# Kernel tuning notes

Measured on AMD Instinct MI355X. Metric: run time of the kernel, lower is better.

The kernel has to match this reference:

```python
import jax, jax.numpy as jnp
import numpy as np

LOG2 = float(np.log(2.0))
NEG_INF = float('-inf')


def log1mexp(x):
    # numerically accurate log(1 - exp(x)) for x < 0
    return jnp.where(x > -LOG2, jnp.log(-jnp.expm1(x)), jnp.log1p(-jnp.exp(x)))


def encode_input_log(pos):
    neg = log1mexp(pos)
    # interleave [pos_i, neg_i] then prepend constants [-inf (log 0), 0 (log 1)]
    result = jnp.stack([pos, neg], axis=1).reshape(-1)
    constants = jnp.array([NEG_INF, 0.0], dtype=pos.dtype)
    return jnp.concatenate([constants, result])


def sum_layer(x, ptrs, csr, n):
    # product node in log semiring: segment-sum of gathered log-values
    return jax.ops.segment_sum(x[ptrs], csr, num_segments=n)


def logsum_layer(x, ptrs, csr, n, epsilon=1e-15):
    # sum node in log semiring: numerically stable segment log-sum-exp
    g = x[ptrs]
    m = jax.lax.stop_gradient(jax.ops.segment_max(g, csr, num_segments=n))
    z = g - m[csr]
    z = jnp.nan_to_num(z, nan=0.0, posinf=jnp.inf, neginf=-jnp.inf)  # (-inf)-(-inf) -> 0
    s = jax.ops.segment_sum(jnp.exp(z), csr, num_segments=n) + epsilon
    return jnp.log(s) + m


def setup_inputs() -> dict:
    key = jax.random.key(0)
    n_vars = 2_000_000
    deg = 4
    Ns = [4_000_000, 2_000_000, 1_000_000, 500_000]
    sizes_in = [2 + 2 * n_vars] + Ns[:-1]
    ks = jax.random.split(key, 1 + len(Ns))
    # log-probabilities strictly in (log eps, log(1-eps)) so log1mexp is finite
    u = jax.random.uniform(ks[0], (n_vars,), dtype=jnp.float32, minval=1e-6, maxval=1.0 - 1e-6)
    inp = {"weights": jnp.log(u)}
    for i, n in enumerate(Ns):
        e = n * deg
        inp[f"ptrs{i}"] = jax.random.randint(ks[i + 1], (e,), 0, sizes_in[i], dtype=jnp.int32)
        inp[f"csr{i}"] = jnp.repeat(jnp.arange(n, dtype=jnp.int32), deg)  # unrolled CSR, fan-in=deg
        inp[f"n{i}"] = n
    return inp


def reference(weights, ptrs0, csr0, ptrs1, csr1, ptrs2, csr2, ptrs3, csr3, n0, n1, n2, n3):
    x = encode_input_log(weights)
    x = sum_layer(x, ptrs0, csr0, n0)      # layer 0: product (even)
    x = logsum_layer(x, ptrs1, csr1, n1)   # layer 1: sum (odd)
    x = sum_layer(x, ptrs2, csr2, n2)      # layer 2: product
    x = logsum_layer(x, ptrs3, csr3, n3)   # layer 3: sum
    return x
```

## Files before the change

### kernel.cpp

```cpp
#include <hip/hip_runtime.h>
#include <math.h>

#define NEG_INF (-INFINITY)

typedef int      v4i __attribute__((ext_vector_type(4)));
typedef float    v4f __attribute__((ext_vector_type(4)));
typedef _Float16 v4h __attribute__((ext_vector_type(4)));

__device__ __forceinline__ float fast_log1mexp(float v) {
    if (v > -0.125f) {
        float e = v * (1.0f + v * (0.5f + v * (0.16666667f + v * 0.041666667f)));
        return __logf(-e);
    }
    return __logf(1.0f - __expf(v));
}

__global__ __launch_bounds__(256) void cvt_kernel(const float* __restrict__ w,
                                                  _Float16* __restrict__ wh, int n) {
    int i = blockIdx.x * blockDim.x + threadIdx.x;
    int n4 = n >> 2;
    if (i < n4) {
        v4f v = reinterpret_cast<const v4f*>(w)[i];
        v4h o;
        o.x = (_Float16)v.x; o.y = (_Float16)v.y;
        o.z = (_Float16)v.z; o.w = (_Float16)v.w;
        reinterpret_cast<v4h*>(wh)[i] = o;
    }
    int base = n4 << 2;
    if (i < (n - base)) wh[base + i] = (_Float16)w[base + i];
}

__device__ __forceinline__ int widx(int p) { int j = (p >> 1) - 1; return j < 0 ? 0 : j; }
__device__ __forceinline__ float fixw(int p, float v) {
    float r = (p & 1) ? fast_log1mexp(v) : v;
    if (p < 2) r = (p == 0) ? NEG_INF : 0.0f;
    return r;
}

__global__ __launch_bounds__(256) void sum4_enc_kernel(const _Float16* __restrict__ wh,
                                                       const v4i* __restrict__ ptrs,
                                                       _Float16* __restrict__ y, int n, int h) {
    int t = blockIdx.x * blockDim.x + threadIdx.x;
    if (t >= h) return;
    int i0 = t, i1 = t + h, i2 = t + 2 * h, i3 = t + 3 * h;
    int c1 = i1 < n ? i1 : 0, c2 = i2 < n ? i2 : 0, c3 = i3 < n ? i3 : 0;
    v4i p0 = __builtin_nontemporal_load(ptrs + i0);
    v4i p1 = __builtin_nontemporal_load(ptrs + c1);
    v4i p2 = __builtin_nontemporal_load(ptrs + c2);
    v4i p3 = __builtin_nontemporal_load(ptrs + c3);
    float g00 = (float)wh[widx(p0.x)], g01 = (float)wh[widx(p0.y)];
    float g02 = (float)wh[widx(p0.z)], g03 = (float)wh[widx(p0.w)];
    float g10 = (float)wh[widx(p1.x)], g11 = (float)wh[widx(p1.y)];
    float g12 = (float)wh[widx(p1.z)], g13 = (float)wh[widx(p1.w)];
    float g20 = (float)wh[widx(p2.x)], g21 = (float)wh[widx(p2.y)];
    float g22 = (float)wh[widx(p2.z)], g23 = (float)wh[widx(p2.w)];
    float g30 = (float)wh[widx(p3.x)], g31 = (float)wh[widx(p3.y)];
    float g32 = (float)wh[widx(p3.z)], g33 = (float)wh[widx(p3.w)];
    float s0 = (fixw(p0.x, g00) + fixw(p0.y, g01)) + (fixw(p0.z, g02) + fixw(p0.w, g03));
    float s1 = (fixw(p1.x, g10) + fixw(p1.y, g11)) + (fixw(p1.z, g12) + fixw(p1.w, g13));
    float s2 = (fixw(p2.x, g20) + fixw(p2.y, g21)) + (fixw(p2.z, g22) + fixw(p2.w, g23));
    float s3 = (fixw(p3.x, g30) + fixw(p3.y, g31)) + (fixw(p3.z, g32) + fixw(p3.w, g33));
    __builtin_nontemporal_store((_Float16)s0, y + i0);
    if (i1 < n) __builtin_nontemporal_store((_Float16)s1, y + i1);
    if (i2 < n) __builtin_nontemporal_store((_Float16)s2, y + i2);
    if (i3 < n) __builtin_nontemporal_store((_Float16)s3, y + i3);
}

__device__ __forceinline__ float lse4(float a, float b, float c, float d) {
    float m = fmaxf(fmaxf(a, b), fmaxf(c, d));
    if (m == NEG_INF) return NEG_INF;
    float s = __expf(a - m) + __expf(b - m) + __expf(c - m) + __expf(d - m) + 1e-15f;
    return __logf(s) + m;
}

__global__ __launch_bounds__(256) void logsum4_l1_kernel(const _Float16* __restrict__ x,
                                                         const v4i* __restrict__ ptrs,
                                                         _Float16* __restrict__ y,
                                                         int n, int h) {
    int t = blockIdx.x * blockDim.x + threadIdx.x;
    if (t >= h) return;
    int i0 = t, i1 = t + h;
    int c1 = i1 < n ? i1 : 0;
    v4i p0 = __builtin_nontemporal_load(ptrs + i0);
    v4i p1 = __builtin_nontemporal_load(ptrs + c1);
    float a0 = (float)x[p0.x], b0 = (float)x[p0.y];
    float e0 = (float)x[p0.z], d0 = (float)x[p0.w];
    float a1 = (float)x[p1.x], b1 = (float)x[p1.y];
    float e1 = (float)x[p1.z], d1 = (float)x[p1.w];
    float s0 = lse4(a0, b0, e0, d0);
    float s1 = lse4(a1, b1, e1, d1);
    __builtin_nontemporal_store((_Float16)s0, y + i0);
    if (i1 < n) __builtin_nontemporal_store((_Float16)s1, y + i1);
}

__global__ __launch_bounds__(256) void sum4_h2h_kernel(const _Float16* __restrict__ x,
                                                       const v4i* __restrict__ ptrs,
                                                       _Float16* __restrict__ y, int n, int h) {
    int t = blockIdx.x * blockDim.x + threadIdx.x;
    if (t >= h) return;
    int i0 = t, i1 = t + h;
    int c1 = i1 < n ? i1 : 0;
    v4i p0 = __builtin_nontemporal_load(ptrs + i0);
    v4i p1 = __builtin_nontemporal_load(ptrs + c1);
    float s0 = ((float)x[p0.x] + (float)x[p0.y]) + ((float)x[p0.z] + (float)x[p0.w]);
    float s1 = ((float)x[p1.x] + (float)x[p1.y]) + ((float)x[p1.z] + (float)x[p1.w]);
    __builtin_nontemporal_store((_Float16)s0, y + i0);
    if (i1 < n) __builtin_nontemporal_store((_Float16)s1, y + i1);
}

__global__ __launch_bounds__(256) void logsum4_h2f_kernel(const _Float16* __restrict__ x,
                                                          const v4i* __restrict__ ptrs,
                                                          float* __restrict__ y, int n) {
    int t = blockIdx.x * blockDim.x + threadIdx.x;
    if (t >= n) return;
    v4i p = __builtin_nontemporal_load(ptrs + t);
    float r = lse4((float)x[p.x], (float)x[p.y], (float)x[p.z], (float)x[p.w]);
    __builtin_nontemporal_store(r, y + t);
}

extern "C" void kernel_launch(void* const* d_in, const int* in_sizes, int n_in,
                              void* d_out, int out_size, void* d_ws, size_t ws_size,
                              hipStream_t stream) {
    const float* w     = (const float*)d_in[0];
    const v4i*   ptrs0 = (const v4i*)d_in[1];
    const v4i*   ptrs1 = (const v4i*)d_in[4];
    const v4i*   ptrs2 = (const v4i*)d_in[7];
    const v4i*   ptrs3 = (const v4i*)d_in[10];

    const int n_vars = in_sizes[0];
    const int n0 = in_sizes[1] / 4;
    const int n1 = in_sizes[4] / 4;
    const int n2 = in_sizes[7] / 4;
    const int n3 = in_sizes[10] / 4;

    char* ws = (char*)d_ws;
    size_t off = 0;
    _Float16* wh = (_Float16*)(ws + off); off += ((size_t)n_vars * 2 + 255) & ~(size_t)255;
    _Float16* y0 = (_Float16*)(ws + off); off += ((size_t)n0 * 2 + 255) & ~(size_t)255;
    _Float16* y1 = (_Float16*)(ws + off); off += ((size_t)n1 * 2 + 255) & ~(size_t)255;
    _Float16* y2 = (_Float16*)(ws + off);
    float* out = (float*)d_out;

    const int B = 256;
    int hc = (n_vars + 3) / 4;
    int h0 = (n0 + 3) / 4;
    int h1 = (n1 + 1) / 2;
    int h2 = (n2 + 1) / 2;

    cvt_kernel        <<<(hc + B - 1) / B, B, 0, stream>>>(w, wh, n_vars);
    sum4_enc_kernel   <<<(h0 + B - 1) / B, B, 0, stream>>>(wh, ptrs0, y0, n0, h0);
    logsum4_l1_kernel <<<(h1 + B - 1) / B, B, 0, stream>>>(y0, ptrs1, y1, n1, h1);
    sum4_h2h_kernel   <<<(h2 + B - 1) / B, B, 0, stream>>>(y1, ptrs2, y2, n2, h2);
    logsum4_h2f_kernel<<<(n3 + B - 1) / B, B, 0, stream>>>(y2, ptrs3, out, n3);
}
```

Measured before the change: 371.1 us.

## Split layer-1 gathers into two index-range passes to improve cache locality

The layer-1 logsum kernel now gives each thread four output nodes instead of two. It gathers inputs in two phases: first only the pointers into the lower half of the layer-0 output, then, after a block barrier, the pointers into the upper half. The two partial log-sum-exps are combined with a merge step. The aim is to keep each phase's random-gather working set (about 4 MB of fp16) resident in cache, in exchange for extra predicated loads and exp/log work, a __syncthreads that only loosely aligns phases across the grid, and launch bounds of 8 waves.

```diff
diff --git a/kernel.cpp b/kernel.cpp
--- a/kernel.cpp
+++ b/kernel.cpp
@@ -66,31 +66,84 @@
     if (i3 < n) __builtin_nontemporal_store((_Float16)s3, y + i3);
 }
 
-__device__ __forceinline__ float lse4(float a, float b, float c, float d) {
+__device__ __forceinline__ float plse4(float a, float b, float c, float d) {
     float m = fmaxf(fmaxf(a, b), fmaxf(c, d));
     if (m == NEG_INF) return NEG_INF;
-    float s = __expf(a - m) + __expf(b - m) + __expf(c - m) + __expf(d - m) + 1e-15f;
+    float s = __expf(a - m) + __expf(b - m) + __expf(c - m) + __expf(d - m);
     return __logf(s) + m;
 }
 
-__global__ __launch_bounds__(256) void logsum4_l1_kernel(const _Float16* __restrict__ x,
-                                                         const v4i* __restrict__ ptrs,
-                                                         _Float16* __restrict__ y,
-                                                         int n, int h) {
-    int t = blockIdx.x * blockDim.x + threadIdx.x;
-    if (t >= h) return;
-    int i0 = t, i1 = t + h;
-    int c1 = i1 < n ? i1 : 0;
+__device__ __forceinline__ float merge_lse(float LA, float LB) {
+    float m = fmaxf(LA, LB);
+    if (m == NEG_INF) return NEG_INF;
+    float s = __expf(LA - m) + __expf(LB - m) + 1e-15f;
+    return __logf(s) + m;
+}
+
+__global__ __launch_bounds__(256, 8) void l1_fused_kernel(const _Float16* __restrict__ x,
+                                                          const v4i* __restrict__ ptrs,
+                                                          _Float16* __restrict__ y,
+                                                          int n, int h, int half) {
+    int t = blockIdx.x * blockDim.x + threadIdx.x;
+    bool act = t < h;
+    int tt = act ? t : 0;
+    int i0 = tt, i1 = tt + h, i2 = tt + 2 * h, i3 = tt + 3 * h;
+    int c1 = i1 < n ? i1 : 0, c2 = i2 < n ? i2 : 0, c3 = i3 < n ? i3 : 0;
     v4i p0 = __builtin_nontemporal_load(ptrs + i0);
     v4i p1 = __builtin_nontemporal_load(ptrs + c1);
-    float a0 = (float)x[p0.x], b0 = (float)x[p0.y];
-    float e0 = (float)x[p0.z], d0 = (float)x[p0.w];
-    float a1 = (float)x[p1.x], b1 = (float)x[p1.y];
-    float e1 = (float)x[p1.z], d1 = (float)x[p1.w];
-    float s0 = lse4(a0, b0, e0, d0);
-    float s1 = lse4(a1, b1, e1, d1);
-    __builtin_nontemporal_store((_Float16)s0, y + i0);
-    if (i1 < n) __builtin_nontemporal_store((_Float16)s1, y + i1);
+    v4i p2 = __builtin_nontemporal_load(ptrs + c2);
+    v4i p3 = __builtin_nontemporal_load(ptrs + c3);
+
+    float a0 = p0.x < half ? (float)x[p0.x] : NEG_INF;
+    float b0 = p0.y < half ? (float)x[p0.y] : NEG_INF;
+    float e0 = p0.z < half ? (float)x[p0.z] : NEG_INF;
+    float d0 = p0.w < half ? (float)x[p0.w] : NEG_INF;
+    float a1 = p1.x < half ? (float)x[p1.x] : NEG_INF;
+    float b1 = p1.y < half ? (float)x[p1.y] : NEG_INF;
+    float e1 = p1.z < half ? (float)x[p1.z] : NEG_INF;
+    float d1 = p1.w < half ? (float)x[p1.w] : NEG_INF;
+    float a2 = p2.x < half ? (float)x[p2.x] : NEG_INF;
+    float b2 = p2.y < half ? (float)x[p2.y] : NEG_INF;
+    float e2 = p2.z < half ? (float)x[p2.z] : NEG_INF;
+    float d2 = p2.w < half ? (float)x[p2.w] : NEG_INF;
+    float a3 = p3.x < half ? (float)x[p3.x] : NEG_INF;
+    float b3 = p3.y < half ? (float)x[p3.y] : NEG_INF;
+    float e3 = p3.z < half ? (float)x[p3.z] : NEG_INF;
+    float d3 = p3.w < half ? (float)x[p3.w] : NEG_INF;
+    float la0 = plse4(a0, b0, e0, d0);
+    float la1 = plse4(a1, b1, e1, d1);
+    float la2 = plse4(a2, b2, e2, d2);
+    float la3 = plse4(a3, b3, e3, d3);
+
+    __syncthreads();
+
+    a0 = p0.x >= half ? (float)x[p0.x] : NEG_INF;
+    b0 = p0.y >= half ? (float)x[p0.y] : NEG_INF;
+    e0 = p0.z >= half ? (float)x[p0.z] : NEG_INF;
+    d0 = p0.w >= half ? (float)x[p0.w] : NEG_INF;
+    a1 = p1.x >= half ? (float)x[p1.x] : NEG_INF;
+    b1 = p1.y >= half ? (float)x[p1.y] : NEG_INF;
+    e1 = p1.z >= half ? (float)x[p1.z] : NEG_INF;
+    d1 = p1.w >= half ? (float)x[p1.w] : NEG_INF;
+    a2 = p2.x >= half ? (float)x[p2.x] : NEG_INF;
+    b2 = p2.y >= half ? (float)x[p2.y] : NEG_INF;
+    e2 = p2.z >= half ? (float)x[p2.z] : NEG_INF;
+    d2 = p2.w >= half ? (float)x[p2.w] : NEG_INF;
+    a3 = p3.x >= half ? (float)x[p3.x] : NEG_INF;
+    b3 = p3.y >= half ? (float)x[p3.y] : NEG_INF;
+    e3 = p3.z >= half ? (float)x[p3.z] : NEG_INF;
+    d3 = p3.w >= half ? (float)x[p3.w] : NEG_INF;
+    float s0 = merge_lse(la0, plse4(a0, b0, e0, d0));
+    float s1 = merge_lse(la1, plse4(a1, b1, e1, d1));
+    float s2 = merge_lse(la2, plse4(a2, b2, e2, d2));
+    float s3 = merge_lse(la3, plse4(a3, b3, e3, d3));
+
+    if (act) {
+        __builtin_nontemporal_store((_Float16)s0, y + i0);
+        if (i1 < n) __builtin_nontemporal_store((_Float16)s1, y + i1);
+        if (i2 < n) __builtin_nontemporal_store((_Float16)s2, y + i2);
+        if (i3 < n) __builtin_nontemporal_store((_Float16)s3, y + i3);
+    }
 }
 
 __global__ __launch_bounds__(256) void sum4_h2h_kernel(const _Float16* __restrict__ x,
@@ -108,6 +161,13 @@
     if (i1 < n) __builtin_nontemporal_store((_Float16)s1, y + i1);
 }
 
+__device__ __forceinline__ float lse4(float a, float b, float c, float d) {
+    float m = fmaxf(fmaxf(a, b), fmaxf(c, d));
+    if (m == NEG_INF) return NEG_INF;
+    float s = __expf(a - m) + __expf(b - m) + __expf(c - m) + __expf(d - m) + 1e-15f;
+    return __logf(s) + m;
+}
+
 __global__ __launch_bounds__(256) void logsum4_h2f_kernel(const _Float16* __restrict__ x,
                                                           const v4i* __restrict__ ptrs,
                                                           float* __restrict__ y, int n) {
@@ -144,12 +204,13 @@
     const int B = 256;
     int hc = (n_vars + 3) / 4;
     int h0 = (n0 + 3) / 4;
-    int h1 = (n1 + 1) / 2;
+    int h1 = (n1 + 3) / 4;
     int h2 = (n2 + 1) / 2;
+    int half0 = n0 / 2;
 
     cvt_kernel        <<<(hc + B - 1) / B, B, 0, stream>>>(w, wh, n_vars);
     sum4_enc_kernel   <<<(h0 + B - 1) / B, B, 0, stream>>>(wh, ptrs0, y0, n0, h0);
-    logsum4_l1_kernel <<<(h1 + B - 1) / B, B, 0, stream>>>(y0, ptrs1, y1, n1, h1);
+    l1_fused_kernel   <<<(h1 + B - 1) / B, B, 0, stream>>>(y0, ptrs1, y1, n1, h1, half0);
     sum4_h2h_kernel   <<<(h2 + B - 1) / B, B, 0, stream>>>(y1, ptrs2, y2, n2, h2);
     logsum4_h2f_kernel<<<(n3 + B - 1) / B, B, 0, stream>>>(y2, ptrs3, out, n3);
 }
```

Measured after the change: 353.8 us. 4.7% less time.

## Fuse all layers into a cooperative persistent kernel with split-half gathers

Applied to the files above, without the earlier changes.

Replaces the five separate layer kernels with one cooperative kernel that uses grid-wide syncs between stages. The sum layer over y0 is split into two passes, each gathering only from one half of y0 and merging partial log-sum-exps, so each pass's gather working set is smaller and more cache-friendly. This removes per-launch overhead and aims to improve cache locality for random gathers. In exchange it adds several grid-wide barriers, doubles gather instruction count in that layer, and limits the grid to the resident block count.

```diff
diff --git a/kernel.cpp b/kernel.cpp
--- a/kernel.cpp
+++ b/kernel.cpp
@@ -1,7 +1,10 @@
 #include <hip/hip_runtime.h>
+#include <hip/hip_cooperative_groups.h>
 #include <math.h>
 
 #define NEG_INF (-INFINITY)
+
+namespace cg = cooperative_groups;
 
 typedef int      v4i __attribute__((ext_vector_type(4)));
 typedef float    v4f __attribute__((ext_vector_type(4)));
@@ -13,21 +16,6 @@
         return __logf(-e);
     }
     return __logf(1.0f - __expf(v));
-}
-
-__global__ __launch_bounds__(256) void cvt_kernel(const float* __restrict__ w,
-                                                  _Float16* __restrict__ wh, int n) {
-    int i = blockIdx.x * blockDim.x + threadIdx.x;
-    int n4 = n >> 2;
-    if (i < n4) {
-        v4f v = reinterpret_cast<const v4f*>(w)[i];
-        v4h o;
-        o.x = (_Float16)v.x; o.y = (_Float16)v.y;
-        o.z = (_Float16)v.z; o.w = (_Float16)v.w;
-        reinterpret_cast<v4h*>(wh)[i] = o;
-    }
-    int base = n4 << 2;
-    if (i < (n - base)) wh[base + i] = (_Float16)w[base + i];
 }
 
 __device__ __forceinline__ int widx(int p) { int j = (p >> 1) - 1; return j < 0 ? 0 : j; }
@@ -37,33 +25,18 @@
     return r;
 }
 
-__global__ __launch_bounds__(256) void sum4_enc_kernel(const _Float16* __restrict__ wh,
-                                                       const v4i* __restrict__ ptrs,
-                                                       _Float16* __restrict__ y, int n, int h) {
-    int t = blockIdx.x * blockDim.x + threadIdx.x;
-    if (t >= h) return;
-    int i0 = t, i1 = t + h, i2 = t + 2 * h, i3 = t + 3 * h;
-    int c1 = i1 < n ? i1 : 0, c2 = i2 < n ? i2 : 0, c3 = i3 < n ? i3 : 0;
-    v4i p0 = __builtin_nontemporal_load(ptrs + i0);
-    v4i p1 = __builtin_nontemporal_load(ptrs + c1);
-    v4i p2 = __builtin_nontemporal_load(ptrs + c2);
-    v4i p3 = __builtin_nontemporal_load(ptrs + c3);
-    float g00 = (float)wh[widx(p0.x)], g01 = (float)wh[widx(p0.y)];
-    float g02 = (float)wh[widx(p0.z)], g03 = (float)wh[widx(p0.w)];
-    float g10 = (float)wh[widx(p1.x)], g11 = (float)wh[widx(p1.y)];
-    float g12 = (float)wh[widx(p1.z)], g13 = (float)wh[widx(p1.w)];
-    float g20 = (float)wh[widx(p2.x)], g21 = (float)wh[widx(p2.y)];
-    float g22 = (float)wh[widx(p2.z)], g23 = (float)wh[widx(p2.w)];
-    float g30 = (float)wh[widx(p3.x)], g31 = (float)wh[widx(p3.y)];
-    float g32 = (float)wh[widx(p3.z)], g33 = (float)wh[widx(p3.w)];
-    float s0 = (fixw(p0.x, g00) + fixw(p0.y, g01)) + (fixw(p0.z, g02) + fixw(p0.w, g03));
-    float s1 = (fixw(p1.x, g10) + fixw(p1.y, g11)) + (fixw(p1.z, g12) + fixw(p1.w, g13));
-    float s2 = (fixw(p2.x, g20) + fixw(p2.y, g21)) + (fixw(p2.z, g22) + fixw(p2.w, g23));
-    float s3 = (fixw(p3.x, g30) + fixw(p3.y, g31)) + (fixw(p3.z, g32) + fixw(p3.w, g33));
-    __builtin_nontemporal_store((_Float16)s0, y + i0);
-    if (i1 < n) __builtin_nontemporal_store((_Float16)s1, y + i1);
-    if (i2 < n) __builtin_nontemporal_store((_Float16)s2, y + i2);
-    if (i3 < n) __builtin_nontemporal_store((_Float16)s3, y + i3);
+__device__ __forceinline__ float plse4(float a, float b, float c, float d) {
+    float m = fmaxf(fmaxf(a, b), fmaxf(c, d));
+    if (m == NEG_INF) return NEG_INF;
+    float s = __expf(a - m) + __expf(b - m) + __expf(c - m) + __expf(d - m);
+    return __logf(s) + m;
+}
+
+__device__ __forceinline__ float merge_lse(float LA, float LB) {
+    float m = fmaxf(LA, LB);
+    if (m == NEG_INF) return NEG_INF;
+    float s = __expf(LA - m) + __expf(LB - m) + 1e-15f;
+    return __logf(s) + m;
 }
 
 __device__ __forceinline__ float lse4(float a, float b, float c, float d) {
@@ -73,49 +46,155 @@
     return __logf(s) + m;
 }
 
-__global__ __launch_bounds__(256) void logsum4_l1_kernel(const _Float16* __restrict__ x,
-                                                         const v4i* __restrict__ ptrs,
-                                                         _Float16* __restrict__ y,
-                                                         int n, int h) {
-    int t = blockIdx.x * blockDim.x + threadIdx.x;
-    if (t >= h) return;
-    int i0 = t, i1 = t + h;
-    int c1 = i1 < n ? i1 : 0;
-    v4i p0 = __builtin_nontemporal_load(ptrs + i0);
-    v4i p1 = __builtin_nontemporal_load(ptrs + c1);
-    float a0 = (float)x[p0.x], b0 = (float)x[p0.y];
-    float e0 = (float)x[p0.z], d0 = (float)x[p0.w];
-    float a1 = (float)x[p1.x], b1 = (float)x[p1.y];
-    float e1 = (float)x[p1.z], d1 = (float)x[p1.w];
-    float s0 = lse4(a0, b0, e0, d0);
-    float s1 = lse4(a1, b1, e1, d1);
-    __builtin_nontemporal_store((_Float16)s0, y + i0);
-    if (i1 < n) __builtin_nontemporal_store((_Float16)s1, y + i1);
-}
-
-__global__ __launch_bounds__(256) void sum4_h2h_kernel(const _Float16* __restrict__ x,
-                                                       const v4i* __restrict__ ptrs,
-                                                       _Float16* __restrict__ y, int n, int h) {
-    int t = blockIdx.x * blockDim.x + threadIdx.x;
-    if (t >= h) return;
-    int i0 = t, i1 = t + h;
-    int c1 = i1 < n ? i1 : 0;
-    v4i p0 = __builtin_nontemporal_load(ptrs + i0);
-    v4i p1 = __builtin_nontemporal_load(ptrs + c1);
-    float s0 = ((float)x[p0.x] + (float)x[p0.y]) + ((float)x[p0.z] + (float)x[p0.w]);
-    float s1 = ((float)x[p1.x] + (float)x[p1.y]) + ((float)x[p1.z] + (float)x[p1.w]);
-    __builtin_nontemporal_store((_Float16)s0, y + i0);
-    if (i1 < n) __builtin_nontemporal_store((_Float16)s1, y + i1);
-}
-
-__global__ __launch_bounds__(256) void logsum4_h2f_kernel(const _Float16* __restrict__ x,
-                                                          const v4i* __restrict__ ptrs,
-                                                          float* __restrict__ y, int n) {
-    int t = blockIdx.x * blockDim.x + threadIdx.x;
-    if (t >= n) return;
-    v4i p = __builtin_nontemporal_load(ptrs + t);
-    float r = lse4((float)x[p.x], (float)x[p.y], (float)x[p.z], (float)x[p.w]);
-    __builtin_nontemporal_store(r, y + t);
+__global__ __launch_bounds__(256, 8) void spn_mega_kernel(
+    const float* __restrict__ w,
+    _Float16* __restrict__ wh,
+    const v4i* __restrict__ ptrs0,
+    _Float16* __restrict__ y0,
+    const v4i* __restrict__ ptrs1,
+    _Float16* __restrict__ y1,
+    const v4i* __restrict__ ptrs2,
+    _Float16* __restrict__ y2,
+    const v4i* __restrict__ ptrs3,
+    float* __restrict__ out,
+    int n_vars, int n0, int n1, int n2, int n3, int half0)
+{
+    cg::grid_group grid = cg::this_grid();
+    const int tid = blockIdx.x * blockDim.x + threadIdx.x;
+    const int NT  = gridDim.x * blockDim.x;
+
+    {
+        int n4 = n_vars >> 2;
+        for (int i = tid; i < n4; i += NT) {
+            v4f v = reinterpret_cast<const v4f*>(w)[i];
+            v4h o;
+            o.x = (_Float16)v.x; o.y = (_Float16)v.y;
+            o.z = (_Float16)v.z; o.w = (_Float16)v.w;
+            reinterpret_cast<v4h*>(wh)[i] = o;
+        }
+        int base = n4 << 2;
+        int rem = n_vars - base;
+        if (tid < rem) wh[base + tid] = (_Float16)w[base + tid];
+    }
+    grid.sync();
+
+    {
+        int h = (n0 + 3) >> 2;
+        for (int t = tid; t < h; t += NT) {
+            int i0 = t, i1 = t + h, i2 = t + 2 * h, i3 = t + 3 * h;
+            int c1 = i1 < n0 ? i1 : 0, c2 = i2 < n0 ? i2 : 0, c3 = i3 < n0 ? i3 : 0;
+            v4i p0 = __builtin_nontemporal_load(ptrs0 + i0);
+            v4i p1 = __builtin_nontemporal_load(ptrs0 + c1);
+            v4i p2 = __builtin_nontemporal_load(ptrs0 + c2);
+            v4i p3 = __builtin_nontemporal_load(ptrs0 + c3);
+            float g00 = (float)wh[widx(p0.x)], g01 = (float)wh[widx(p0.y)];
+            float g02 = (float)wh[widx(p0.z)], g03 = (float)wh[widx(p0.w)];
+            float g10 = (float)wh[widx(p1.x)], g11 = (float)wh[widx(p1.y)];
+            float g12 = (float)wh[widx(p1.z)], g13 = (float)wh[widx(p1.w)];
+            float g20 = (float)wh[widx(p2.x)], g21 = (float)wh[widx(p2.y)];
+            float g22 = (float)wh[widx(p2.z)], g23 = (float)wh[widx(p2.w)];
+            float g30 = (float)wh[widx(p3.x)], g31 = (float)wh[widx(p3.y)];
+            float g32 = (float)wh[widx(p3.z)], g33 = (float)wh[widx(p3.w)];
+            float s0 = (fixw(p0.x, g00) + fixw(p0.y, g01)) + (fixw(p0.z, g02) + fixw(p0.w, g03));
+            float s1 = (fixw(p1.x, g10) + fixw(p1.y, g11)) + (fixw(p1.z, g12) + fixw(p1.w, g13));
+            float s2 = (fixw(p2.x, g20) + fixw(p2.y, g21)) + (fixw(p2.z, g22) + fixw(p2.w, g23));
+            float s3 = (fixw(p3.x, g30) + fixw(p3.y, g31)) + (fixw(p3.z, g32) + fixw(p3.w, g33));
+            __builtin_nontemporal_store((_Float16)s0, y0 + i0);
+            if (i1 < n0) __builtin_nontemporal_store((_Float16)s1, y0 + i1);
+            if (i2 < n0) __builtin_nontemporal_store((_Float16)s2, y0 + i2);
+            if (i3 < n0) __builtin_nontemporal_store((_Float16)s3, y0 + i3);
+        }
+    }
+    grid.sync();
+
+    {
+        int h = (n1 + 3) >> 2;
+        int chunks = (h + NT - 1) / NT;
+        for (int c = 0; c < chunks; ++c) {
+            int vt = c * NT + tid;
+            bool act = vt < h;
+            int tt = act ? vt : 0;
+            int i0 = tt, i1 = tt + h, i2 = tt + 2 * h, i3 = tt + 3 * h;
+            int c1 = i1 < n1 ? i1 : 0, c2 = i2 < n1 ? i2 : 0, c3 = i3 < n1 ? i3 : 0;
+            v4i p0 = __builtin_nontemporal_load(ptrs1 + i0);
+            v4i p1 = __builtin_nontemporal_load(ptrs1 + c1);
+            v4i p2 = __builtin_nontemporal_load(ptrs1 + c2);
+            v4i p3 = __builtin_nontemporal_load(ptrs1 + c3);
+
+            float a0 = p0.x < half0 ? (float)y0[p0.x] : NEG_INF;
+            float b0 = p0.y < half0 ? (float)y0[p0.y] : NEG_INF;
+            float e0 = p0.z < half0 ? (float)y0[p0.z] : NEG_INF;
+            float d0 = p0.w < half0 ? (float)y0[p0.w] : NEG_INF;
+            float a1 = p1.x < half0 ? (float)y0[p1.x] : NEG_INF;
+            float b1 = p1.y < half0 ? (float)y0[p1.y] : NEG_INF;
+            float e1 = p1.z < half0 ? (float)y0[p1.z] : NEG_INF;
+            float d1 = p1.w < half0 ? (float)y0[p1.w] : NEG_INF;
+            float a2 = p2.x < half0 ? (float)y0[p2.x] : NEG_INF;
+            float b2 = p2.y < half0 ? (float)y0[p2.y] : NEG_INF;
+            float e2 = p2.z < half0 ? (float)y0[p2.z] : NEG_INF;
+            float d2 = p2.w < half0 ? (float)y0[p2.w] : NEG_INF;
+            float a3 = p3.x < half0 ? (float)y0[p3.x] : NEG_INF;
+            float b3 = p3.y < half0 ? (float)y0[p3.y] : NEG_INF;
+            float e3 = p3.z < half0 ? (float)y0[p3.z] : NEG_INF;
+            float d3 = p3.w < half0 ? (float)y0[p3.w] : NEG_INF;
+            float la0 = plse4(a0, b0, e0, d0);
+            float la1 = plse4(a1, b1, e1, d1);
+            float la2 = plse4(a2, b2, e2, d2);
+            float la3 = plse4(a3, b3, e3, d3);
+
+            grid.sync();
+
+            a0 = p0.x >= half0 ? (float)y0[p0.x] : NEG_INF;
+            b0 = p0.y >= half0 ? (float)y0[p0.y] : NEG_INF;
+            e0 = p0.z >= half0 ? (float)y0[p0.z] : NEG_INF;
+            d0 = p0.w >= half0 ? (float)y0[p0.w] : NEG_INF;
+            a1 = p1.x >= half0 ? (float)y0[p1.x] : NEG_INF;
+            b1 = p1.y >= half0 ? (float)y0[p1.y] : NEG_INF;
+            e1 = p1.z >= half0 ? (float)y0[p1.z] : NEG_INF;
+            d1 = p1.w >= half0 ? (float)y0[p1.w] : NEG_INF;
+            a2 = p2.x >= half0 ? (float)y0[p2.x] : NEG_INF;
+            b2 = p2.y >= half0 ? (float)y0[p2.y] : NEG_INF;
+            e2 = p2.z >= half0 ? (float)y0[p2.z] : NEG_INF;
+            d2 = p2.w >= half0 ? (float)y0[p2.w] : NEG_INF;
+            a3 = p3.x >= half0 ? (float)y0[p3.x] : NEG_INF;
+            b3 = p3.y >= half0 ? (float)y0[p3.y] : NEG_INF;
+            e3 = p3.z >= half0 ? (float)y0[p3.z] : NEG_INF;
+            d3 = p3.w >= half0 ? (float)y0[p3.w] : NEG_INF;
+            float s0 = merge_lse(la0, plse4(a0, b0, e0, d0));
+            float s1 = merge_lse(la1, plse4(a1, b1, e1, d1));
+            float s2 = merge_lse(la2, plse4(a2, b2, e2, d2));
+            float s3 = merge_lse(la3, plse4(a3, b3, e3, d3));
+
+            if (act) {
+                __builtin_nontemporal_store((_Float16)s0, y1 + i0);
+                if (i1 < n1) __builtin_nontemporal_store((_Float16)s1, y1 + i1);
+                if (i2 < n1) __builtin_nontemporal_store((_Float16)s2, y1 + i2);
+                if (i3 < n1) __builtin_nontemporal_store((_Float16)s3, y1 + i3);
+            }
+            grid.sync();
+        }
+    }
+
+    {
+        int h = (n2 + 1) >> 1;
+        for (int t = tid; t < h; t += NT) {
+            int i0 = t, i1 = t + h;
+            int c1 = i1 < n2 ? i1 : 0;
+            v4i p0 = __builtin_nontemporal_load(ptrs2 + i0);
+            v4i p1 = __builtin_nontemporal_load(ptrs2 + c1);
+            float s0 = ((float)y1[p0.x] + (float)y1[p0.y]) + ((float)y1[p0.z] + (float)y1[p0.w]);
+            float s1 = ((float)y1[p1.x] + (float)y1[p1.y]) + ((float)y1[p1.z] + (float)y1[p1.w]);
+            __builtin_nontemporal_store((_Float16)s0, y2 + i0);
+            if (i1 < n2) __builtin_nontemporal_store((_Float16)s1, y2 + i1);
+        }
+    }
+    grid.sync();
+
+    for (int t = tid; t < n3; t += NT) {
+        v4i p = __builtin_nontemporal_load(ptrs3 + t);
+        float r = lse4((float)y2[p.x], (float)y2[p.y], (float)y2[p.z], (float)y2[p.w]);
+        __builtin_nontemporal_store(r, out + t);
+    }
 }
 
 extern "C" void kernel_launch(void* const* d_in, const int* in_sizes, int n_in,
@@ -127,11 +206,11 @@
     const v4i*   ptrs2 = (const v4i*)d_in[7];
     const v4i*   ptrs3 = (const v4i*)d_in[10];
 
-    const int n_vars = in_sizes[0];
-    const int n0 = in_sizes[1] / 4;
-    const int n1 = in_sizes[4] / 4;
-    const int n2 = in_sizes[7] / 4;
-    const int n3 = in_sizes[10] / 4;
+    int n_vars = in_sizes[0];
+    int n0 = in_sizes[1] / 4;
+    int n1 = in_sizes[4] / 4;
+    int n2 = in_sizes[7] / 4;
+    int n3 = in_sizes[10] / 4;
 
     char* ws = (char*)d_ws;
     size_t off = 0;
@@ -141,15 +220,31 @@
     _Float16* y2 = (_Float16*)(ws + off);
     float* out = (float*)d_out;
 
-    const int B = 256;
-    int hc = (n_vars + 3) / 4;
-    int h0 = (n0 + 3) / 4;
-    int h1 = (n1 + 1) / 2;
-    int h2 = (n2 + 1) / 2;
-
-    cvt_kernel        <<<(hc + B - 1) / B, B, 0, stream>>>(w, wh, n_vars);
-    sum4_enc_kernel   <<<(h0 + B - 1) / B, B, 0, stream>>>(wh, ptrs0, y0, n0, h0);
-    logsum4_l1_kernel <<<(h1 + B - 1) / B, B, 0, stream>>>(y0, ptrs1, y1, n1, h1);
-    sum4_h2h_kernel   <<<(h2 + B - 1) / B, B, 0, stream>>>(y1, ptrs2, y2, n2, h2);
-    logsum4_h2f_kernel<<<(n3 + B - 1) / B, B, 0, stream>>>(y2, ptrs3, out, n3);
-}
+    int half0 = n0 / 2;
+
+    static int nblk = 0;
+    if (nblk == 0) {
+        int perCU = 0;
+        if (hipOccupancyMaxActiveBlocksPerMultiprocessor(
+                &perCU, reinterpret_cast<const void*>(spn_mega_kernel), 256, 0) != hipSuccess ||
+            perCU <= 0)
+            perCU = 8;
+        int cus = 0;
+        if (hipDeviceGetAttribute(&cus, hipDeviceAttributeMultiprocessorCount, 0) != hipSuccess ||
+            cus <= 0)
+            cus = 256;
+        nblk = perCU * cus;
+        if (nblk > 2048) nblk = 2048;
+    }
+
+    void* args[] = {
+        (void*)&w, (void*)&wh,
+        (void*)&ptrs0, (void*)&y0,
+        (void*)&ptrs1, (void*)&y1,
+        (void*)&ptrs2, (void*)&y2,
+        (void*)&ptrs3, (void*)&out,
+        (void*)&n_vars, (void*)&n0, (void*)&n1, (void*)&n2, (void*)&n3, (void*)&half0
+    };
+    hipLaunchCooperativeKernel(reinterpret_cast<const void*>(spn_mega_kernel),
+                               dim3(nblk), dim3(256), args, 0, stream);
+}
```

New measurement: 1.252 ms. 237% more time.

## Process contiguous output nodes per thread and split layer-1 gathers by source half

Applied to the files above, without the earlier changes.

Each thread now handles four (or two) consecutive output nodes, so it reads a contiguous run of pointer vectors and writes one vectorized fp16 or fp32 store instead of strided scalar stores. The layer-1 sum kernel is restructured into two passes. The first gathers only sources in the lower half of the input array and the second only the upper half, with a block barrier between them. The two partial log-sum-exps are then merged. The aim is to shrink each pass's gather working set so it fits better in cache, at the cost of doubled gather instructions, extra exp/log work, and a barrier.

```diff
diff --git a/kernel.cpp b/kernel.cpp
--- a/kernel.cpp
+++ b/kernel.cpp
@@ -6,6 +6,8 @@
 typedef int      v4i __attribute__((ext_vector_type(4)));
 typedef float    v4f __attribute__((ext_vector_type(4)));
 typedef _Float16 v4h __attribute__((ext_vector_type(4)));
+typedef _Float16 v2h __attribute__((ext_vector_type(2)));
+typedef float    v2f __attribute__((ext_vector_type(2)));
 
 __device__ __forceinline__ float fast_log1mexp(float v) {
     if (v > -0.125f) {
@@ -42,12 +44,14 @@
                                                        _Float16* __restrict__ y, int n, int h) {
     int t = blockIdx.x * blockDim.x + threadIdx.x;
     if (t >= h) return;
-    int i0 = t, i1 = t + h, i2 = t + 2 * h, i3 = t + 3 * h;
-    int c1 = i1 < n ? i1 : 0, c2 = i2 < n ? i2 : 0, c3 = i3 < n ? i3 : 0;
-    v4i p0 = __builtin_nontemporal_load(ptrs + i0);
-    v4i p1 = __builtin_nontemporal_load(ptrs + c1);
-    v4i p2 = __builtin_nontemporal_load(ptrs + c2);
-    v4i p3 = __builtin_nontemporal_load(ptrs + c3);
+    int base = t << 2;
+    int b1 = base + 1 < n ? base + 1 : 0;
+    int b2 = base + 2 < n ? base + 2 : 0;
+    int b3 = base + 3 < n ? base + 3 : 0;
+    v4i p0 = __builtin_nontemporal_load(ptrs + base);
+    v4i p1 = __builtin_nontemporal_load(ptrs + b1);
+    v4i p2 = __builtin_nontemporal_load(ptrs + b2);
+    v4i p3 = __builtin_nontemporal_load(ptrs + b3);
     float g00 = (float)wh[widx(p0.x)], g01 = (float)wh[widx(p0.y)];
     float g02 = (float)wh[widx(p0.z)], g03 = (float)wh[widx(p0.w)];
     float g10 = (float)wh[widx(p1.x)], g11 = (float)wh[widx(p1.y)];
@@ -60,10 +64,114 @@
     float s1 = (fixw(p1.x, g10) + fixw(p1.y, g11)) + (fixw(p1.z, g12) + fixw(p1.w, g13));
     float s2 = (fixw(p2.x, g20) + fixw(p2.y, g21)) + (fixw(p2.z, g22) + fixw(p2.w, g23));
     float s3 = (fixw(p3.x, g30) + fixw(p3.y, g31)) + (fixw(p3.z, g32) + fixw(p3.w, g33));
-    __builtin_nontemporal_store((_Float16)s0, y + i0);
-    if (i1 < n) __builtin_nontemporal_store((_Float16)s1, y + i1);
-    if (i2 < n) __builtin_nontemporal_store((_Float16)s2, y + i2);
-    if (i3 < n) __builtin_nontemporal_store((_Float16)s3, y + i3);
+    if (base + 3 < n) {
+        v4h o; o.x = (_Float16)s0; o.y = (_Float16)s1; o.z = (_Float16)s2; o.w = (_Float16)s3;
+        __builtin_nontemporal_store(o, reinterpret_cast<v4h*>(y + base));
+    } else {
+        y[base] = (_Float16)s0;
+        if (base + 1 < n) y[base + 1] = (_Float16)s1;
+        if (base + 2 < n) y[base + 2] = (_Float16)s2;
+    }
+}
+
+__device__ __forceinline__ float plse4(float a, float b, float c, float d) {
+    float m = fmaxf(fmaxf(a, b), fmaxf(c, d));
+    if (m == NEG_INF) return NEG_INF;
+    float s = __expf(a - m) + __expf(b - m) + __expf(c - m) + __expf(d - m);
+    return __logf(s) + m;
+}
+
+__device__ __forceinline__ float merge_lse(float LA, float LB) {
+    float m = fmaxf(LA, LB);
+    if (m == NEG_INF) return NEG_INF;
+    float s = __expf(LA - m) + __expf(LB - m) + 1e-15f;
+    return __logf(s) + m;
+}
+
+__device__ __forceinline__ float gsel_lo(const _Float16* __restrict__ x, int p, int half) {
+    int q = p < half ? p : 0;
+    float v = (float)x[q];
+    return p < half ? v : NEG_INF;
+}
+__device__ __forceinline__ float gsel_hi(const _Float16* __restrict__ x, int p, int half) {
+    int q = p >= half ? p : half;
+    float v = (float)x[q];
+    return p >= half ? v : NEG_INF;
+}
+
+__global__ __launch_bounds__(256) void l1_fused_kernel(const _Float16* __restrict__ x,
+                                                       const v4i* __restrict__ ptrs,
+                                                       _Float16* __restrict__ y,
+                                                       int n, int h, int half) {
+    int t = blockIdx.x * blockDim.x + threadIdx.x;
+    bool act = t < h;
+    int tt = act ? t : 0;
+    int base = tt << 2;
+    int b1 = base + 1 < n ? base + 1 : 0;
+    int b2 = base + 2 < n ? base + 2 : 0;
+    int b3 = base + 3 < n ? base + 3 : 0;
+    v4i p0 = __builtin_nontemporal_load(ptrs + base);
+    v4i p1 = __builtin_nontemporal_load(ptrs + b1);
+    v4i p2 = __builtin_nontemporal_load(ptrs + b2);
+    v4i p3 = __builtin_nontemporal_load(ptrs + b3);
+
+    float la0 = plse4(gsel_lo(x, p0.x, half), gsel_lo(x, p0.y, half),
+                      gsel_lo(x, p0.z, half), gsel_lo(x, p0.w, half));
+    float la1 = plse4(gsel_lo(x, p1.x, half), gsel_lo(x, p1.y, half),
+                      gsel_lo(x, p1.z, half), gsel_lo(x, p1.w, half));
+    float la2 = plse4(gsel_lo(x, p2.x, half), gsel_lo(x, p2.y, half),
+                      gsel_lo(x, p2.z, half), gsel_lo(x, p2.w, half));
+    float la3 = plse4(gsel_lo(x, p3.x, half), gsel_lo(x, p3.y, half),
+                      gsel_lo(x, p3.z, half), gsel_lo(x, p3.w, half));
+
+    __syncthreads();
+
+    float s0 = merge_lse(la0, plse4(gsel_hi(x, p0.x, half), gsel_hi(x, p0.y, half),
+                                    gsel_hi(x, p0.z, half), gsel_hi(x, p0.w, half)));
+    float s1 = merge_lse(la1, plse4(gsel_hi(x, p1.x, half), gsel_hi(x, p1.y, half),
+                                    gsel_hi(x, p1.z, half), gsel_hi(x, p1.w, half)));
+    float s2 = merge_lse(la2, plse4(gsel_hi(x, p2.x, half), gsel_hi(x, p2.y, half),
+                                    gsel_hi(x, p2.z, half), gsel_hi(x, p2.w, half)));
+    float s3 = merge_lse(la3, plse4(gsel_hi(x, p3.x, half), gsel_hi(x, p3.y, half),
+                                    gsel_hi(x, p3.z, half), gsel_hi(x, p3.w, half)));
+
+    if (act) {
+        if (base + 3 < n) {
+            v4h o; o.x = (_Float16)s0; o.y = (_Float16)s1; o.z = (_Float16)s2; o.w = (_Float16)s3;
+            __builtin_nontemporal_store(o, reinterpret_cast<v4h*>(y + base));
+        } else {
+            y[base] = (_Float16)s0;
+            if (base + 1 < n) y[base + 1] = (_Float16)s1;
+            if (base + 2 < n) y[base + 2] = (_Float16)s2;
+        }
+    }
+}
+
+__global__ __launch_bounds__(256) void sum4_h2h_kernel(const _Float16* __restrict__ x,
+                                                       const v4i* __restrict__ ptrs,
+                                                       _Float16* __restrict__ y, int n, int h) {
+    int t = blockIdx.x * blockDim.x + threadIdx.x;
+    if (t >= h) return;
+    int base = t << 2;
+    int b1 = base + 1 < n ? base + 1 : 0;
+    int b2 = base + 2 < n ? base + 2 : 0;
+    int b3 = base + 3 < n ? base + 3 : 0;
+    v4i p0 = __builtin_nontemporal_load(ptrs + base);
+    v4i p1 = __builtin_nontemporal_load(ptrs + b1);
+    v4i p2 = __builtin_nontemporal_load(ptrs + b2);
+    v4i p3 = __builtin_nontemporal_load(ptrs + b3);
+    float s0 = ((float)x[p0.x] + (float)x[p0.y]) + ((float)x[p0.z] + (float)x[p0.w]);
+    float s1 = ((float)x[p1.x] + (float)x[p1.y]) + ((float)x[p1.z] + (float)x[p1.w]);
+    float s2 = ((float)x[p2.x] + (float)x[p2.y]) + ((float)x[p2.z] + (float)x[p2.w]);
+    float s3 = ((float)x[p3.x] + (float)x[p3.y]) + ((float)x[p3.z] + (float)x[p3.w]);
+    if (base + 3 < n) {
+        v4h o; o.x = (_Float16)s0; o.y = (_Float16)s1; o.z = (_Float16)s2; o.w = (_Float16)s3;
+        __builtin_nontemporal_store(o, reinterpret_cast<v4h*>(y + base));
+    } else {
+        y[base] = (_Float16)s0;
+        if (base + 1 < n) y[base + 1] = (_Float16)s1;
+        if (base + 2 < n) y[base + 2] = (_Float16)s2;
+    }
 }
 
 __device__ __forceinline__ float lse4(float a, float b, float c, float d) {
@@ -73,49 +181,23 @@
     return __logf(s) + m;
 }
 
-__global__ __launch_bounds__(256) void logsum4_l1_kernel(const _Float16* __restrict__ x,
-                                                         const v4i* __restrict__ ptrs,
-                                                         _Float16* __restrict__ y,
-                                                         int n, int h) {
-    int t = blockIdx.x * blockDim.x + threadIdx.x;
-    if (t >= h) return;
-    int i0 = t, i1 = t + h;
-    int c1 = i1 < n ? i1 : 0;
-    v4i p0 = __builtin_nontemporal_load(ptrs + i0);
-    v4i p1 = __builtin_nontemporal_load(ptrs + c1);
-    float a0 = (float)x[p0.x], b0 = (float)x[p0.y];
-    float e0 = (float)x[p0.z], d0 = (float)x[p0.w];
-    float a1 = (float)x[p1.x], b1 = (float)x[p1.y];
-    float e1 = (float)x[p1.z], d1 = (float)x[p1.w];
-    float s0 = lse4(a0, b0, e0, d0);
-    float s1 = lse4(a1, b1, e1, d1);
-    __builtin_nontemporal_store((_Float16)s0, y + i0);
-    if (i1 < n) __builtin_nontemporal_store((_Float16)s1, y + i1);
-}
-
-__global__ __launch_bounds__(256) void sum4_h2h_kernel(const _Float16* __restrict__ x,
-                                                       const v4i* __restrict__ ptrs,
-                                                       _Float16* __restrict__ y, int n, int h) {
-    int t = blockIdx.x * blockDim.x + threadIdx.x;
-    if (t >= h) return;
-    int i0 = t, i1 = t + h;
-    int c1 = i1 < n ? i1 : 0;
-    v4i p0 = __builtin_nontemporal_load(ptrs + i0);
-    v4i p1 = __builtin_nontemporal_load(ptrs + c1);
-    float s0 = ((float)x[p0.x] + (float)x[p0.y]) + ((float)x[p0.z] + (float)x[p0.w]);
-    float s1 = ((float)x[p1.x] + (float)x[p1.y]) + ((float)x[p1.z] + (float)x[p1.w]);
-    __builtin_nontemporal_store((_Float16)s0, y + i0);
-    if (i1 < n) __builtin_nontemporal_store((_Float16)s1, y + i1);
-}
-
 __global__ __launch_bounds__(256) void logsum4_h2f_kernel(const _Float16* __restrict__ x,
                                                           const v4i* __restrict__ ptrs,
-                                                          float* __restrict__ y, int n) {
-    int t = blockIdx.x * blockDim.x + threadIdx.x;
-    if (t >= n) return;
-    v4i p = __builtin_nontemporal_load(ptrs + t);
-    float r = lse4((float)x[p.x], (float)x[p.y], (float)x[p.z], (float)x[p.w]);
-    __builtin_nontemporal_store(r, y + t);
+                                                          float* __restrict__ y, int n, int h) {
+    int t = blockIdx.x * blockDim.x + threadIdx.x;
+    if (t >= h) return;
+    int base = t << 1;
+    int b1 = base + 1 < n ? base + 1 : 0;
+    v4i p0 = __builtin_nontemporal_load(ptrs + base);
+    v4i p1 = __builtin_nontemporal_load(ptrs + b1);
+    float r0 = lse4((float)x[p0.x], (float)x[p0.y], (float)x[p0.z], (float)x[p0.w]);
+    float r1 = lse4((float)x[p1.x], (float)x[p1.y], (float)x[p1.z], (float)x[p1.w]);
+    if (base + 1 < n) {
+        v2f o; o.x = r0; o.y = r1;
+        __builtin_nontemporal_store(o, reinterpret_cast<v2f*>(y + base));
+    } else {
+        y[base] = r0;
+    }
 }
 
 extern "C" void kernel_launch(void* const* d_in, const int* in_sizes, int n_in,
@@ -144,12 +226,14 @@
     const int B = 256;
     int hc = (n_vars + 3) / 4;
     int h0 = (n0 + 3) / 4;
-    int h1 = (n1 + 1) / 2;
-    int h2 = (n2 + 1) / 2;
+    int h1 = (n1 + 3) / 4;
+    int h2 = (n2 + 3) / 4;
+    int h3 = (n3 + 1) / 2;
+    int half0 = n0 / 2;
 
     cvt_kernel        <<<(hc + B - 1) / B, B, 0, stream>>>(w, wh, n_vars);
     sum4_enc_kernel   <<<(h0 + B - 1) / B, B, 0, stream>>>(wh, ptrs0, y0, n0, h0);
-    logsum4_l1_kernel <<<(h1 + B - 1) / B, B, 0, stream>>>(y0, ptrs1, y1, n1, h1);
+    l1_fused_kernel   <<<(h1 + B - 1) / B, B, 0, stream>>>(y0, ptrs1, y1, n1, h1, half0);
     sum4_h2h_kernel   <<<(h2 + B - 1) / B, B, 0, stream>>>(y1, ptrs2, y2, n2, h2);
-    logsum4_h2f_kernel<<<(n3 + B - 1) / B, B, 0, stream>>>(y2, ptrs3, out, n3);
-}
+    logsum4_h2f_kernel<<<(h3 + B - 1) / B, B, 0, stream>>>(y2, ptrs3, out, n3, h3);
+}
```

After: 387.7 us. 1.04x slower.
